# Kernel optimization log

Measured on AMD Instinct MI355X. Metric: run time of the kernel, lower is better.

The kernel has to match this reference:

```python
import jax, jax.numpy as jnp
import numpy as np

D_MODEL = 1024
N_HEADS = 16
HEAD_DIM = D_MODEL // N_HEADS


def setup_inputs() -> dict:
    key = jax.random.key(0)
    k_x, k_w1, k_b1, k_w2, k_b2 = jax.random.split(key, 5)
    B, S = 4, 2048
    x = jax.random.normal(k_x, (B, S, D_MODEL), dtype=jnp.float32)
    # torch Linear init ~ U(-1/sqrt(fan_in), 1/sqrt(fan_in))
    lim = 1.0 / np.sqrt(D_MODEL)
    qkv_w = jax.random.uniform(k_w1, (D_MODEL, 3 * D_MODEL), jnp.float32, -lim, lim)
    qkv_b = jax.random.uniform(k_b1, (3 * D_MODEL,), jnp.float32, -lim, lim)
    out_w = jax.random.uniform(k_w2, (D_MODEL, D_MODEL), jnp.float32, -lim, lim)
    out_b = jax.random.uniform(k_b2, (D_MODEL,), jnp.float32, -lim, lim)
    return {"x": x, "qkv_w": qkv_w, "qkv_b": qkv_b, "out_w": out_w, "out_b": out_b}


def reference(x, qkv_w, qkv_b, out_w, out_b):
    B, S, D = x.shape
    scale = HEAD_DIM ** -0.5
    qkv = x @ qkv_w + qkv_b  # [B,S,3D]
    q, k, v = jnp.split(qkv, 3, axis=-1)
    def to_heads(t):
        return t.reshape(B, S, N_HEADS, HEAD_DIM).transpose(0, 2, 1, 3)  # [B,H,S,Dh]
    q, k, v = to_heads(q), to_heads(k), to_heads(v)
    scores = jnp.einsum('bhqd,bhkd->bhqk', q, k) * scale  # [B,H,S,S]
    causal = jnp.tril(jnp.ones((S, S), dtype=bool))
    scores = jnp.where(causal, scores, -jnp.inf)
    weights = jax.nn.softmax(scores, axis=-1)  # dropout is identity in eval
    out = jnp.einsum('bhqk,bhkd->bhqd', weights, v)  # [B,H,S,Dh]
    out = out.transpose(0, 2, 1, 3).reshape(B, S, D)
    return out @ out_w + out_b
```

## Files before the change

kernel.cpp:

```cpp
#include <hip/hip_runtime.h>

typedef __bf16 bf16x8 __attribute__((ext_vector_type(8)));
typedef float f32x4 __attribute__((ext_vector_type(4)));
typedef unsigned short u16;

#define D_MODEL 1024
#define SEQ     2048
#define BATCH   4
#define NH      16
#define DH      64

static __device__ __forceinline__ u16 f2bf(float f) {
    union { float f; unsigned u; } v; v.f = f;
    unsigned r = v.u + 0x7FFF + ((v.u >> 16) & 1);
    return (u16)(r >> 16);
}
static __device__ __forceinline__ void storeC(u16* C, size_t off, float v) { C[off] = f2bf(v); }
static __device__ __forceinline__ void storeC(float* C, size_t off, float v) { C[off] = v; }

static __device__ __forceinline__ void async_ld16(u16* lds, const u16* g) {
    __builtin_amdgcn_global_load_lds(
        (const __attribute__((address_space(1))) unsigned int*)g,
        (__attribute__((address_space(3))) unsigned int*)lds, 16, 0, 0);
}

__global__ __launch_bounds__(256) void cvt_bf16(const float* __restrict__ in,
                                                u16* __restrict__ out) {
    size_t i = ((size_t)blockIdx.x * 256 + threadIdx.x) * 8;
    float4 a = *(const float4*)(in + i);
    float4 b = *(const float4*)(in + i + 4);
    u16 t[8] = {f2bf(a.x), f2bf(a.y), f2bf(a.z), f2bf(a.w),
                f2bf(b.x), f2bf(b.y), f2bf(b.z), f2bf(b.w)};
    *(uint4*)(out + i) = *(uint4*)t;
}

__global__ void transpose_w(const float* __restrict__ in, u16* __restrict__ out,
                            int K, int N) {
    __shared__ float tile[32][33];
    int n0 = blockIdx.x * 32, k0 = blockIdx.y * 32;
    int tx = threadIdx.x, ty = threadIdx.y;
    for (int i = ty; i < 32; i += 8)
        tile[i][tx] = in[(size_t)(k0 + i) * N + n0 + tx];
    __syncthreads();
    for (int i = ty; i < 32; i += 8)
        out[(size_t)(n0 + i) * K + k0 + tx] = f2bf(tile[tx][i]);
}

template <typename CT>
__global__ __launch_bounds__(256) void gemm_bt(
    const u16* __restrict__ A, int lda,
    const u16* __restrict__ Bt, int ldb,
    const float* __restrict__ bias,
    CT* __restrict__ C, int ldc, int K) {
    __shared__ u16 As[2][128 * 64];
    __shared__ u16 Bs[2][128 * 64];
    int m0 = blockIdx.x * 128, n0 = blockIdx.y * 128;
    int tid = threadIdx.x;
    int w = tid >> 6, lane = tid & 63, l15 = lane & 15, g = lane >> 4;
    int wm = (w & 1) * 64, wn = (w >> 1) * 64;
    int srow = w * 8 + (lane >> 3);
    int sk8  = lane & 7;

    auto stage = [&](int buf, int kt) {
        #pragma unroll
        for (int p = 0; p < 4; ++p) {
            int row = p * 32 + srow;
            int k8 = sk8 ^ (row & 7);
            async_ld16(&As[buf][p * 2048 + w * 512],
                       A + (size_t)(m0 + row) * lda + kt + k8 * 8);
            async_ld16(&Bs[buf][p * 2048 + w * 512],
                       Bt + (size_t)(n0 + row) * ldb + kt + k8 * 8);
        }
    };

    f32x4 acc[4][4] = {};

    stage(0, 0);
    __syncthreads();
    for (int kt = 0; kt < K; kt += 64) {
        int cur = (kt >> 6) & 1;
        if (kt + 64 < K) stage(cur ^ 1, kt + 64);
        #pragma unroll
        for (int kk = 0; kk < 2; ++kk) {
            bf16x8 af[4], bf_[4];
            int s8 = ((kk << 2) | g) ^ (l15 & 7);
            #pragma unroll
            for (int i = 0; i < 4; ++i) {
                af[i]  = *(const bf16x8*)&As[cur][(wm + i * 16 + l15) * 64 + s8 * 8];
                bf_[i] = *(const bf16x8*)&Bs[cur][(wn + i * 16 + l15) * 64 + s8 * 8];
            }
            #pragma unroll
            for (int i = 0; i < 4; ++i)
                #pragma unroll
                for (int j = 0; j < 4; ++j)
                    acc[i][j] = __builtin_amdgcn_mfma_f32_16x16x32_bf16(
                        af[i], bf_[j], acc[i][j], 0, 0, 0);
        }
        __syncthreads();
    }
    #pragma unroll
    for (int j = 0; j < 4; ++j) {
        int n = n0 + wn + j * 16 + l15;
        float bv = bias[n];
        #pragma unroll
        for (int i = 0; i < 4; ++i) {
            int mbase = m0 + wm + i * 16 + g * 4;
            #pragma unroll
            for (int r = 0; r < 4; ++r)
                storeC(C, (size_t)(mbase + r) * ldc + n, acc[i][j][r] + bv);
        }
    }
}

__global__ __launch_bounds__(256) void gemm_qkv(
    const u16* __restrict__ A,
    const u16* __restrict__ Bt,
    const float* __restrict__ bias,
    u16* __restrict__ Qd, u16* __restrict__ pkK, u16* __restrict__ pkV) {
    __shared__ u16 As[2][128 * 64];
    __shared__ u16 Bs[2][128 * 64];
    const int K = D_MODEL;
    int m0 = blockIdx.x * 128, n0 = blockIdx.y * 128;
    int tid = threadIdx.x;
    int w = tid >> 6, lane = tid & 63, l15 = lane & 15, g = lane >> 4;
    int wm = (w & 1) * 64, wn = (w >> 1) * 64;
    int srow = w * 8 + (lane >> 3);
    int sk8  = lane & 7;

    auto stage = [&](int buf, int kt) {
        #pragma unroll
        for (int p = 0; p < 4; ++p) {
            int row = p * 32 + srow;
            int k8 = sk8 ^ (row & 7);
            async_ld16(&As[buf][p * 2048 + w * 512],
                       A + (size_t)(m0 + row) * K + kt + k8 * 8);
            async_ld16(&Bs[buf][p * 2048 + w * 512],
                       Bt + (size_t)(n0 + row) * K + kt + k8 * 8);
        }
    };

    f32x4 acc[4][4] = {};

    stage(0, 0);
    __syncthreads();
    for (int kt = 0; kt < K; kt += 64) {
        int cur = (kt >> 6) & 1;
        if (kt + 64 < K) stage(cur ^ 1, kt + 64);
        #pragma unroll
        for (int kk = 0; kk < 2; ++kk) {
            bf16x8 af[4], bf_[4];
            int s8 = ((kk << 2) | g) ^ (l15 & 7);
            #pragma unroll
            for (int i = 0; i < 4; ++i) {
                af[i]  = *(const bf16x8*)&As[cur][(wm + i * 16 + l15) * 64 + s8 * 8];
                bf_[i] = *(const bf16x8*)&Bs[cur][(wn + i * 16 + l15) * 64 + s8 * 8];
            }
            #pragma unroll
            for (int i = 0; i < 4; ++i)
                #pragma unroll
                for (int j = 0; j < 4; ++j)
                    acc[i][j] = __builtin_amdgcn_mfma_f32_16x16x32_bf16(
                        af[i], bf_[j], acc[i][j], 0, 0, 0);
        }
        __syncthreads();
    }
    #pragma unroll
    for (int j = 0; j < 4; ++j) {
        int n = n0 + wn + j * 16 + l15;
        float bv = bias[n];
        int region = n >> 10;
        int hd = n & 1023;
        int h = hd >> 6, d = hd & 63;
        #pragma unroll
        for (int i = 0; i < 4; ++i) {
            #pragma unroll
            for (int r = 0; r < 4; ++r) {
                int m = m0 + wm + i * 16 + g * 4 + r;
                u16 vb = f2bf(acc[i][j][r] + bv);
                int b = m >> 11, s = m & 2047;
                int t = s >> 6, kap = s & 63;
                if (region == 0) {
                    Qd[(size_t)m * 1024 + hd] = vb;
                } else if (region == 1) {
                    int bh = b * 16 + h;
                    int nb = kap >> 4, lk = kap & 15;
                    int kk = d >> 5, gk = (d >> 3) & 3, jk = d & 7;
                    pkK[(size_t)(bh * 32 + t) * 4096 +
                        ((nb * 2 + kk) * 64 + gk * 16 + lk) * 8 + jk] = vb;
                } else {
                    int bh = b * 16 + h;
                    int kk = kap >> 5, gv = (kap >> 3) & 3, jv = kap & 7;
                    int nb = d >> 4, lv = d & 15;
                    pkV[(size_t)(bh * 32 + t) * 4096 +
                        ((nb * 2 + kk) * 64 + gv * 16 + lv) * 8 + jv] = vb;
                }
            }
        }
    }
}

__global__ __launch_bounds__(256) void attn_flash(
    u16* __restrict__ Qd, const u16* __restrict__ pkK,
    const u16* __restrict__ pkV) {
    __shared__ __align__(16) char smemraw[18432 + 256];
    u16 (*Pt)[32][72] = (u16(*)[32][72])smemraw;
    float* Om = (float*)smemraw;
    float* Lm = (float*)(smemraw + 18432);

    int bh = blockIdx.x, b = bh >> 4, h = bh & 15;
    int tid = threadIdx.x;
    int w = tid >> 6, lane = tid & 63, l15 = lane & 15, g = lane >> 4;
    int wq = w >> 1, wk = w & 1;

    const u16* Kb = pkK + (size_t)bh * 32 * 4096;
    const u16* Vb = pkV + (size_t)bh * 32 * 4096;
    u16* Qbase = Qd + (size_t)b * SEQ * 1024 + h * DH;

    int qts[2] = {31 - (int)blockIdx.y, (int)blockIdx.y};

    #pragma unroll
    for (int qi = 0; qi < 2; ++qi) {
        int qt = qts[qi];
        int q0 = qt * 64;

        bf16x8 qfrag[2][2];
        #pragma unroll
        for (int st = 0; st < 2; ++st) {
            const u16* qp = Qbase + (size_t)(q0 + wq * 32 + st * 16 + l15) * 1024 + g * 8;
            bf16x8 a = *(const bf16x8*)qp;
            bf16x8 c = *(const bf16x8*)(qp + 32);
            #pragma unroll
            for (int jj = 0; jj < 8; ++jj) {
                a[jj] = (__bf16)((float)a[jj] * 0.125f);
                c[jj] = (__bf16)((float)c[jj] * 0.125f);
            }
            qfrag[st][0] = a; qfrag[st][1] = c;
        }

        f32x4 o[2][4] = {};
        float lsum[2][4] = {};

        for (int t = wk; t <= qt; t += 2) {
            const u16* kt = Kb + t * 4096;
            const u16* vt = Vb + t * 4096;
            bf16x8 kf[4][2], vf[4][2];
            #pragma unroll
            for (int nb = 0; nb < 4; ++nb) {
                #pragma unroll
                for (int kk = 0; kk < 2; ++kk) {
                    kf[nb][kk] = *(const bf16x8*)(kt + ((nb * 2 + kk) * 64 + lane) * 8);
                    vf[nb][kk] = *(const bf16x8*)(vt + ((nb * 2 + kk) * 64 + lane) * 8);
                }
            }
            bool diag = (t == qt);
            int k0 = t * 64;

            #pragma unroll
            for (int st = 0; st < 2; ++st) {
                f32x4 s[4] = {};
                #pragma unroll
                for (int nb = 0; nb < 4; ++nb)
                    #pragma unroll
                    for (int kk = 0; kk < 2; ++kk)
                        s[nb] = __builtin_amdgcn_mfma_f32_16x16x32_bf16(
                            qfrag[st][kk], kf[nb][kk], s[nb], 0, 0, 0);

                #pragma unroll
                for (int r = 0; r < 4; ++r) {
                    int qg = q0 + wq * 32 + st * 16 + g * 4 + r;
                    #pragma unroll
                    for (int nb = 0; nb < 4; ++nb) {
                        float p = __expf(s[nb][r]);
                        if (diag && (k0 + nb * 16 + l15) > qg) p = 0.f;
                        lsum[st][r] += p;
                        Pt[w][st * 16 + g * 4 + r][nb * 16 + l15] =
                            (u16)(__float_as_uint(p) >> 16);
                    }
                }

                #pragma unroll
                for (int kk = 0; kk < 2; ++kk) {
                    bf16x8 aP = *(const bf16x8*)&Pt[w][st * 16 + l15][kk * 32 + g * 8];
                    #pragma unroll
                    for (int nb = 0; nb < 4; ++nb)
                        o[st][nb] = __builtin_amdgcn_mfma_f32_16x16x32_bf16(
                            aP, vf[nb][kk], o[st][nb], 0, 0, 0);
                }
            }
        }

        #pragma unroll
        for (int msk = 1; msk < 16; msk <<= 1)
            #pragma unroll
            for (int st = 0; st < 2; ++st)
                #pragma unroll
                for (int r = 0; r < 4; ++r)
                    lsum[st][r] += __shfl_xor(lsum[st][r], msk, 64);

        __syncthreads();
        if (wk == 0) {
            #pragma unroll
            for (int st = 0; st < 2; ++st)
                #pragma unroll
                for (int r = 0; r < 4; ++r) {
                    int qrow = wq * 32 + st * 16 + g * 4 + r;
                    if (l15 == 0) Lm[qrow] = lsum[st][r];
                    #pragma unroll
                    for (int nb = 0; nb < 4; ++nb)
                        Om[qrow * 65 + nb * 16 + l15] = o[st][nb][r];
                }
        }
        __syncthreads();
        if (wk == 1) {
            #pragma unroll
            for (int st = 0; st < 2; ++st)
                #pragma unroll
                for (int r = 0; r < 4; ++r) {
                    int qrow = wq * 32 + st * 16 + g * 4 + r;
                    float inv = 1.f / (lsum[st][r] + Lm[qrow]);
                    u16* op = Qbase + (size_t)(q0 + qrow) * 1024;
                    #pragma unroll
                    for (int nb = 0; nb < 4; ++nb) {
                        float val = (o[st][nb][r] + Om[qrow * 65 + nb * 16 + l15]) * inv;
                        op[nb * 16 + l15] = f2bf(val);
                    }
                }
        }
        __syncthreads();
    }
}

extern "C" void kernel_launch(void* const* d_in, const int* in_sizes, int n_in,
                              void* d_out, int out_size, void* d_ws, size_t ws_size,
                              hipStream_t stream) {
    const float* x     = (const float*)d_in[0];
    const float* qkv_w = (const float*)d_in[1];
    const float* qkv_b = (const float*)d_in[2];
    const float* out_w = (const float*)d_in[3];
    const float* out_b = (const float*)d_in[4];
    float* out = (float*)d_out;

    const int M = BATCH * SEQ;
    u16* Qd     = (u16*)d_ws;
    u16* pkK    = Qd  + (size_t)M * D_MODEL;
    u16* pkV    = pkK + (size_t)64 * 32 * 4096;
    u16* xb     = pkV + (size_t)64 * 32 * 4096;
    u16* Wqkv_t = xb  + (size_t)M * D_MODEL;
    u16* Wout_t = Wqkv_t + (size_t)3 * D_MODEL * D_MODEL;

    cvt_bf16<<<(size_t)M * D_MODEL / (256 * 8), 256, 0, stream>>>(x, xb);
    transpose_w<<<dim3(3 * D_MODEL / 32, D_MODEL / 32), dim3(32, 8), 0, stream>>>(
        qkv_w, Wqkv_t, D_MODEL, 3 * D_MODEL);
    transpose_w<<<dim3(D_MODEL / 32, D_MODEL / 32), dim3(32, 8), 0, stream>>>(
        out_w, Wout_t, D_MODEL, D_MODEL);

    gemm_qkv<<<dim3(M / 128, 3 * D_MODEL / 128), 256, 0, stream>>>(
        xb, Wqkv_t, qkv_b, Qd, pkK, pkV);

    attn_flash<<<dim3(BATCH * NH, SEQ / 64 / 2), 256, 0, stream>>>(Qd, pkK, pkV);

    gemm_bt<float><<<dim3(M / 128, D_MODEL / 128), 256, 0, stream>>>(
        Qd, D_MODEL, Wout_t, D_MODEL, out_b, out, D_MODEL, D_MODEL);
}
```

Before: 255.9 us.

## Merge prepass kernels, fold softmax scale into Q, use exp2, split diagonal tile

```diff
diff --git a/kernel.cpp b/kernel.cpp
--- a/kernel.cpp
+++ b/kernel.cpp
@@ -10,6 +10,8 @@
 #define NH      16
 #define DH      64
 
+#define QSCALE 0.18033688011f
+
 static __device__ __forceinline__ u16 f2bf(float f) {
     union { float f; unsigned u; } v; v.f = f;
     unsigned r = v.u + 0x7FFF + ((v.u >> 16) & 1);
@@ -24,26 +26,39 @@
         (__attribute__((address_space(3))) unsigned int*)lds, 16, 0, 0);
 }
 
-__global__ __launch_bounds__(256) void cvt_bf16(const float* __restrict__ in,
-                                                u16* __restrict__ out) {
-    size_t i = ((size_t)blockIdx.x * 256 + threadIdx.x) * 8;
-    float4 a = *(const float4*)(in + i);
-    float4 b = *(const float4*)(in + i + 4);
-    u16 t[8] = {f2bf(a.x), f2bf(a.y), f2bf(a.z), f2bf(a.w),
-                f2bf(b.x), f2bf(b.y), f2bf(b.z), f2bf(b.w)};
-    *(uint4*)(out + i) = *(uint4*)t;
-}
-
-__global__ void transpose_w(const float* __restrict__ in, u16* __restrict__ out,
-                            int K, int N) {
+__global__ __launch_bounds__(256) void prepass(
+    const float* __restrict__ x,     u16* __restrict__ xb,
+    const float* __restrict__ qkv_w, u16* __restrict__ Wqkv_t,
+    const float* __restrict__ out_w, u16* __restrict__ Wout_t) {
     __shared__ float tile[32][33];
-    int n0 = blockIdx.x * 32, k0 = blockIdx.y * 32;
-    int tx = threadIdx.x, ty = threadIdx.y;
+    int bid = blockIdx.x, tid = threadIdx.x;
+
+    if (bid < 4096) {
+        size_t i = ((size_t)bid * 256 + tid) * 8;
+        float4 a = *(const float4*)(x + i);
+        float4 b = *(const float4*)(x + i + 4);
+        u16 t[8] = {f2bf(a.x), f2bf(a.y), f2bf(a.z), f2bf(a.w),
+                    f2bf(b.x), f2bf(b.y), f2bf(b.z), f2bf(b.w)};
+        *(uint4*)(xb + i) = *(uint4*)t;
+        return;
+    }
+
+    const float* in; u16* out; int n0, k0, N;
+    if (bid < 7168) {
+        int bb = bid - 4096;
+        n0 = (bb % 96) * 32; k0 = (bb / 96) * 32;
+        in = qkv_w; out = Wqkv_t; N = 3 * D_MODEL;
+    } else {
+        int bb = bid - 7168;
+        n0 = (bb & 31) * 32; k0 = (bb >> 5) * 32;
+        in = out_w; out = Wout_t; N = D_MODEL;
+    }
+    int tx = tid & 31, ty = tid >> 5;
     for (int i = ty; i < 32; i += 8)
         tile[i][tx] = in[(size_t)(k0 + i) * N + n0 + tx];
     __syncthreads();
     for (int i = ty; i < 32; i += 8)
-        out[(size_t)(n0 + i) * K + k0 + tx] = f2bf(tile[tx][i]);
+        out[(size_t)(n0 + i) * D_MODEL + k0 + tx] = f2bf(tile[tx][i]);
 }
 
 template <typename CT>
@@ -176,23 +191,23 @@
             #pragma unroll
             for (int r = 0; r < 4; ++r) {
                 int m = m0 + wm + i * 16 + g * 4 + r;
-                u16 vb = f2bf(acc[i][j][r] + bv);
+                float fv = acc[i][j][r] + bv;
                 int b = m >> 11, s = m & 2047;
                 int t = s >> 6, kap = s & 63;
                 if (region == 0) {
-                    Qd[(size_t)m * 1024 + hd] = vb;
+                    Qd[(size_t)m * 1024 + hd] = f2bf(fv * QSCALE);
                 } else if (region == 1) {
                     int bh = b * 16 + h;
                     int nb = kap >> 4, lk = kap & 15;
                     int kk = d >> 5, gk = (d >> 3) & 3, jk = d & 7;
                     pkK[(size_t)(bh * 32 + t) * 4096 +
-                        ((nb * 2 + kk) * 64 + gk * 16 + lk) * 8 + jk] = vb;
+                        ((nb * 2 + kk) * 64 + gk * 16 + lk) * 8 + jk] = f2bf(fv);
                 } else {
                     int bh = b * 16 + h;
                     int kk = kap >> 5, gv = (kap >> 3) & 3, jv = kap & 7;
                     int nb = d >> 4, lv = d & 15;
                     pkV[(size_t)(bh * 32 + t) * 4096 +
-                        ((nb * 2 + kk) * 64 + gv * 16 + lv) * 8 + jv] = vb;
+                        ((nb * 2 + kk) * 64 + gv * 16 + lv) * 8 + jv] = f2bf(fv);
                 }
             }
         }
@@ -227,20 +242,14 @@
         #pragma unroll
         for (int st = 0; st < 2; ++st) {
             const u16* qp = Qbase + (size_t)(q0 + wq * 32 + st * 16 + l15) * 1024 + g * 8;
-            bf16x8 a = *(const bf16x8*)qp;
-            bf16x8 c = *(const bf16x8*)(qp + 32);
-            #pragma unroll
-            for (int jj = 0; jj < 8; ++jj) {
-                a[jj] = (__bf16)((float)a[jj] * 0.125f);
-                c[jj] = (__bf16)((float)c[jj] * 0.125f);
-            }
-            qfrag[st][0] = a; qfrag[st][1] = c;
+            qfrag[st][0] = *(const bf16x8*)qp;
+            qfrag[st][1] = *(const bf16x8*)(qp + 32);
         }
 
         f32x4 o[2][4] = {};
         float lsum[2][4] = {};
 
-        for (int t = wk; t <= qt; t += 2) {
+        auto ktile = [&](int t, bool diag) {
             const u16* kt = Kb + t * 4096;
             const u16* vt = Vb + t * 4096;
             bf16x8 kf[4][2], vf[4][2];
@@ -252,7 +261,6 @@
                     vf[nb][kk] = *(const bf16x8*)(vt + ((nb * 2 + kk) * 64 + lane) * 8);
                 }
             }
-            bool diag = (t == qt);
             int k0 = t * 64;
 
             #pragma unroll
@@ -270,7 +278,7 @@
                     int qg = q0 + wq * 32 + st * 16 + g * 4 + r;
                     #pragma unroll
                     for (int nb = 0; nb < 4; ++nb) {
-                        float p = __expf(s[nb][r]);
+                        float p = __builtin_amdgcn_exp2f(s[nb][r]);
                         if (diag && (k0 + nb * 16 + l15) > qg) p = 0.f;
                         lsum[st][r] += p;
                         Pt[w][st * 16 + g * 4 + r][nb * 16 + l15] =
@@ -287,7 +295,10 @@
                             aP, vf[nb][kk], o[st][nb], 0, 0, 0);
                 }
             }
-        }
+        };
+
+        for (int t = wk; t < qt; t += 2) ktile(t, false);
+        if ((qt & 1) == wk) ktile(qt, true);
 
         #pragma unroll
         for (int msk = 1; msk < 16; msk <<= 1)
@@ -348,11 +359,7 @@
     u16* Wqkv_t = xb  + (size_t)M * D_MODEL;
     u16* Wout_t = Wqkv_t + (size_t)3 * D_MODEL * D_MODEL;
 
-    cvt_bf16<<<(size_t)M * D_MODEL / (256 * 8), 256, 0, stream>>>(x, xb);
-    transpose_w<<<dim3(3 * D_MODEL / 32, D_MODEL / 32), dim3(32, 8), 0, stream>>>(
-        qkv_w, Wqkv_t, D_MODEL, 3 * D_MODEL);
-    transpose_w<<<dim3(D_MODEL / 32, D_MODEL / 32), dim3(32, 8), 0, stream>>>(
-        out_w, Wout_t, D_MODEL, D_MODEL);
+    prepass<<<dim3(8192), 256, 0, stream>>>(x, xb, qkv_w, Wqkv_t, out_w, Wout_t);
 
     gemm_qkv<<<dim3(M / 128, 3 * D_MODEL / 128), 256, 0, stream>>>(
         xb, Wqkv_t, qkv_b, Qd, pkK, pkV);
```

After: 253.4 us. No clear change (-1.0%).
